# Kernel tuning notes

Measured on AMD Instinct MI355X. Metric: run time of the kernel, lower is better.

The kernel has to match this reference:

```python
import jax, jax.numpy as jnp
from jax import lax
import numpy as np

_LEVELS = [6 * 2 ** i for i in range(1, 8)]  # Dense size per block: 12..768
_LOG_2PI = float(np.log(2.0 * np.pi))


def _expm(A):
    # Differentiable matrix exponential: scaling-and-squaring + Taylor.
    K = 6
    A = A / (2.0 ** K)
    n = A.shape[-1]
    out = jnp.eye(n, dtype=A.dtype)
    term = out
    for j in range(1, 14):
        term = (term @ A) / j
        out = out + term
    for _ in range(K):
        out = out @ out
    return out


def _s2d(x):
    # tf.nn.space_to_depth, block_size=2, NHWC layout (channel order i*2*C+j*C+c)
    B, H, W, C = x.shape
    x = x.reshape(B, H // 2, 2, W // 2, 2, C).transpose(0, 1, 3, 2, 4, 5)
    return x.reshape(B, H // 2, W // 2, 4 * C)


def _block_inverse(y, M, eb, cw, cb, dw, db):
    # inverse of Block = Chain([Dense(s), RealNVP(s//2, shift-only)])
    # Dense inverse: expm(-M) @ (y - bias)
    x = jnp.einsum('ij,bhwj->bhwi', _expm(-M), y - eb)
    d = M.shape[0] // 2
    x0, x1 = x[..., :d], x[..., d:]
    # shift_and_log_scale: Dense(zeros-init) o relu(Conv2D(256,3,same)); scale=None
    h = jax.nn.relu(lax.conv_general_dilated(
        x0, cw, (1, 1), 'SAME', dimension_numbers=('NHWC', 'HWIO', 'NHWC')) + cb)
    shift = jnp.einsum('bhwk,kd->bhwd', h, dw) + db
    return jnp.concatenate([x0, x1 - shift], axis=-1)


def _log_prob(sample, params):
    x = sample
    ildj = jnp.zeros((), sample.dtype)
    for i, p in enumerate(params):  # levels i=1..7, applied in inverse order
        x = _s2d(x)                 # [B, 256/2^i, 256/2^i, 3*4^i]
        s = _LEVELS[i]
        blk = _block_inverse(x[..., :s], *p)
        x = blk if x.shape[-1] == s else jnp.concatenate([blk, x[..., s:]], axis=-1)
        H = x.shape[1]
        # Faithful to source: the Inline bijector's inverse_log_det_jacobian fn
        # literally returns exp(trace(M)) (a constant-Jacobian scalar), which TFP
        # reduces over the excess spatial event dims => multiply by H*W.
        ildj = ildj + jnp.exp(jnp.trace(p[0])) * (H * H)
    z = x.reshape(x.shape[0], -1)   # Reshape bijector inverse: flatten event
    N = z.shape[-1]
    base = -0.5 * jnp.sum(z * z, axis=-1) - 0.5 * N * _LOG_2PI
    return base + ildj


def setup_inputs() -> dict:
    key = jax.random.key(0)
    inp = {'sample': jax.random.normal(jax.random.fold_in(key, 0), (8, 256, 256, 3), jnp.float32)}
    for i in range(1, 8):
        s = 6 * 2 ** i
        d = s // 2
        ks = jax.random.split(jax.random.fold_in(key, i), 3)
        inp[f'M{i}'] = 0.05 * jax.random.normal(ks[0], (s, s), jnp.float32)
        inp[f'eb{i}'] = jnp.zeros((s,), jnp.float32)
        inp[f'cw{i}'] = jax.random.normal(ks[1], (3, 3, d, 256), jnp.float32) / np.sqrt(9.0 * d)
        inp[f'cb{i}'] = jnp.zeros((256,), jnp.float32)
        inp[f'dw{i}'] = 0.01 * jax.random.normal(ks[2], (256, d), jnp.float32)
        inp[f'db{i}'] = jnp.zeros((d,), jnp.float32)
    return inp


def reference(sample, M1, eb1, cw1, cb1, dw1, db1, M2, eb2, cw2, cb2, dw2, db2,
              M3, eb3, cw3, cb3, dw3, db3, M4, eb4, cw4, cb4, dw4, db4,
              M5, eb5, cw5, cb5, dw5, db5, M6, eb6, cw6, cb6, dw6, db6,
              M7, eb7, cw7, cb7, dw7, db7):
    params = [
        (M1, eb1, cw1, cb1, dw1, db1), (M2, eb2, cw2, cb2, dw2, db2),
        (M3, eb3, cw3, cb3, dw3, db3), (M4, eb4, cw4, cb4, dw4, db4),
        (M5, eb5, cw5, cb5, dw5, db5), (M6, eb6, cw6, cb6, dw6, db6),
        (M7, eb7, cw7, cb7, dw7, db7),
    ]
    return _log_prob(sample, params)
```

## Files before the change

### kernel.cpp

```cpp
#include <hip/hip_runtime.h>
#include <hip/hip_bf16.h>
#include <math.h>


#define NXEL 1572864

typedef __attribute__((ext_vector_type(8))) short bf16x8;
typedef __attribute__((ext_vector_type(4))) float f32x4;

__device__ inline unsigned pkbf(float a, float b) {
  union { __hip_bfloat16 h; unsigned short u; } ca, cb2;
  ca.h = __float2bfloat16(a);
  cb2.h = __float2bfloat16(b);
  return (unsigned)ca.u | ((unsigned)cb2.u << 16);
}

__global__ __launch_bounds__(256) void prep_all_kernel(
    const float* __restrict__ M1, const float* __restrict__ M2,
    const float* __restrict__ M3, const float* __restrict__ M4,
    const float* __restrict__ M5, const float* __restrict__ M6,
    const float* __restrict__ M7, const float* __restrict__ cw1,
    const float* __restrict__ cw2, const float* __restrict__ dw1,
    const float* __restrict__ dw2, float* __restrict__ MT,
    __hip_bfloat16* __restrict__ MTB, float* __restrict__ TR,
    __hip_bfloat16* __restrict__ CWT1, __hip_bfloat16* __restrict__ CWT2,
    __hip_bfloat16* __restrict__ DWT1, __hip_bfloat16* __restrict__ DWT2) {
  int bid = blockIdx.x, tid = threadIdx.x;
  if (bid < 48) {
    int idx = bid * 256 + tid;
    if (idx < 12240) {
      const int cum[5] = {0, 144, 720, 3024, 12240};
      int l = 0;
      while (idx >= cum[l + 1]) l++;
      int local = idx - cum[l];
      int s = 12 << l;
      int k = local / s, c = local - k * s;
      const float* Mp = l == 0 ? M1 : l == 1 ? M2 : l == 2 ? M3 : M4;
      MT[idx] = -Mp[c * s + k];
    }
  } else if (bid < 3072) {
    int idx = (bid - 48) * 256 + tid;
    if (idx < 774144) {
      const int cum[4] = {0, 36864, 184320, 774144};
      int l = 0;
      while (idx >= cum[l + 1]) l++;
      const float* Mp = l == 0 ? M5 : l == 1 ? M6 : M7;
      MTB[idx] = __float2bfloat16(-Mp[idx - cum[l]]);
    }
  } else if (bid < 3079) {
    __shared__ float red[256];
    int l = bid - 3072;
    const float* Mp = l == 0 ? M1 : l == 1 ? M2 : l == 2 ? M3 : l == 3 ? M4
                    : l == 4 ? M5 : l == 5 ? M6 : M7;
    int s = 12 << l;
    float su = 0.f;
    for (int i = tid; i < s; i += 256) su += Mp[(long)i * s + i];
    red[tid] = su;
    __syncthreads();
    for (int st = 128; st > 0; st >>= 1) {
      if (tid < st) red[tid] += red[tid + st];
      __syncthreads();
    }
    if (tid == 0) TR[l] = red[0];
  } else if (bid < 3143) {
    int idx = (bid - 3079) * 256 + tid;
    int n = idx >> 6, k = idx & 63;
    CWT1[idx] = __float2bfloat16(k < 54 ? cw1[k * 256 + n] : 0.f);
  } else if (bid < 3271) {
    int idx = (bid - 3143) * 256 + tid;
    int n = idx >> 7, k = idx & 127;
    CWT2[idx] = __float2bfloat16(k < 108 ? cw2[k * 256 + n] : 0.f);
  } else if (bid < 3287) {
    int idx = (bid - 3271) * 256 + tid;
    int c = idx >> 8, k = idx & 255;
    DWT1[idx] = __float2bfloat16(c < 6 ? dw1[k * 6 + c] : 0.f);
  } else {
    int idx = (bid - 3287) * 256 + tid;
    int c = idx >> 8, k = idx & 255;
    DWT2[idx] = __float2bfloat16(c < 12 ? dw2[k * 12 + c] : 0.f);
  }
}

__global__ __launch_bounds__(256) void expm_apply_kernel(
    const float* __restrict__ prev, const float* __restrict__ Mt,
    const float* __restrict__ eb, float* __restrict__ xblk,
    int s, int Cp, int h, int J, int tvs) {
  extern __shared__ float lds[];
  float* MtS = lds;
  float* Tb = lds + s * s;
  for (int i = threadIdx.x; i < s * s; i += 256) MtS[i] = Mt[i];

  int TV = 1 << tvs;
  int v = threadIdx.x >> tvs;
  int p = threadIdx.x & (TV - 1);
  int c0 = p * 6;
  int NV = 256 >> tvs;
  int sp = s + 1;
  int vec = blockIdx.x * NV + v;
  int hw = h * h;
  int b = vec / hw, rem = vec - b * hw;
  int y = rem / h, x = rem - (rem / h) * h;
  int W2 = 2 * h;
  long rowbase = ((long)(b * W2 + 2 * y) * W2 + 2 * x) * Cp;

  float acc[6];
#pragma unroll
  for (int m = 0; m < 6; m++) {
    int c = c0 + m;
    int q = c / Cp, cp = c - q * Cp;
    float xv = prev[rowbase + (long)((q >> 1) * W2 + (q & 1)) * Cp + cp] - eb[c];
    acc[m] = xv;
    Tb[v * sp + c0 + m] = xv;
  }
  __syncthreads();

  for (int j = 1; j <= J; j++) {
    float inv = 1.0f / (float)j;
    float tn[6] = {0.f, 0.f, 0.f, 0.f, 0.f, 0.f};
    const float* Trow = Tb + v * sp;
    for (int k = 0; k < s; k++) {
      float tv = Trow[k];
      const float* mrow = MtS + k * s + c0;
#pragma unroll
      for (int m = 0; m < 6; m++) tn[m] = fmaf(mrow[m], tv, tn[m]);
    }
    __syncthreads();
#pragma unroll
    for (int m = 0; m < 6; m++) {
      float t2 = tn[m] * inv;
      acc[m] += t2;
      Tb[v * sp + c0 + m] = t2;
    }
    __syncthreads();
  }

  float* xo = xblk + (long)vec * s;
#pragma unroll
  for (int m = 0; m < 6; m++) xo[c0 + m] = acc[m];
}

template <int S>
__global__ __launch_bounds__(S, 2) void expm_chain_kernel(
    const float* __restrict__ prev, const __hip_bfloat16* __restrict__ Mrow,
    const float* __restrict__ eb, float* __restrict__ xblk,
    int Cp, int h, int J) {
  constexpr int NU4 = S / 8;
  __shared__ float tbuf[2][S];
  int c = threadIdx.x;
  int vec = blockIdx.x;
  int hw = h * h, W2 = 2 * h;
  int b = vec / hw, rem = vec - b * hw;
  int y = rem / h, x = rem - (rem / h) * h;
  int q = c / Cp, cp = c - q * Cp;
  long a = ((long)(b * W2 + 2 * y + (q >> 1)) * W2 + 2 * x + (q & 1)) * Cp + cp;

  uint4 mreg[NU4];
  const uint4* rp = (const uint4*)(Mrow + (long)c * S);
#pragma unroll
  for (int k8 = 0; k8 < NU4; k8++) mreg[k8] = rp[k8];

  float v = prev[a] - eb[c];
  float acc = v;
  tbuf[0][c] = v;
  __syncthreads();

  int cur = 0;
  for (int j = 1; j <= J; j++) {
    float inv = 1.0f / (float)j;
    float sacc[4] = {0.f, 0.f, 0.f, 0.f};
    const float* t = tbuf[cur];
#pragma unroll
    for (int k8 = 0; k8 < NU4; k8++) {
      uint4 u = mreg[k8];
      const float* tt = t + (k8 << 3);
      float ss = sacc[k8 & 3];
      ss = fmaf(__uint_as_float(u.x << 16), tt[0], ss);
      ss = fmaf(__uint_as_float(u.x & 0xffff0000u), tt[1], ss);
      ss = fmaf(__uint_as_float(u.y << 16), tt[2], ss);
      ss = fmaf(__uint_as_float(u.y & 0xffff0000u), tt[3], ss);
      ss = fmaf(__uint_as_float(u.z << 16), tt[4], ss);
      ss = fmaf(__uint_as_float(u.z & 0xffff0000u), tt[5], ss);
      ss = fmaf(__uint_as_float(u.w << 16), tt[6], ss);
      ss = fmaf(__uint_as_float(u.w & 0xffff0000u), tt[7], ss);
      sacc[k8 & 3] = ss;
    }
    float tn = ((sacc[0] + sacc[1]) + (sacc[2] + sacc[3])) * inv;
    acc += tn;
    cur ^= 1;
    tbuf[cur][c] = tn;
    __syncthreads();
  }
  xblk[(long)vec * S + c] = acc;
}

__global__ __launch_bounds__(64) void expm_init_kernel(
    const float* __restrict__ prev, const float* __restrict__ eb,
    float* __restrict__ tcur, float* __restrict__ acc, int s, int Cp, int h,
    int nvec) {
  int total = nvec * s;
  int hw = h * h, W2 = 2 * h;
  for (int idx = blockIdx.x * 64 + threadIdx.x; idx < total;
       idx += gridDim.x * 64) {
    int v = idx / s, c = idx - (idx / s) * s;
    int b = v / hw, rem = v - b * hw;
    int y = rem / h, x = rem - (rem / h) * h;
    int q = c / Cp, cp = c - q * Cp;
    long a = ((long)(b * W2 + 2 * y + (q >> 1)) * W2 + 2 * x + (q & 1)) * Cp + cp;
    float xv = prev[a] - eb[c];
    tcur[idx] = xv;
    acc[idx] = xv;
  }
}

template <int S>
__global__ __launch_bounds__(64) void taylor_term_kernel(
    const __hip_bfloat16* __restrict__ Mrow, const float* __restrict__ t_old,
    float* __restrict__ t_new, float* __restrict__ acc, float inv_j) {
  __shared__ float tv[S];
  int tid = threadIdx.x;
  int v = blockIdx.y;
  int c = blockIdx.x * 64 + tid;
  const float4* t4 = (const float4*)(t_old + (long)v * S);
  float4* l4 = (float4*)tv;
  for (int i = tid; i < S / 4; i += 64) l4[i] = t4[i];
  __syncthreads();

  const uint4* rp = (const uint4*)(Mrow + (long)c * S);
  float sacc[4] = {0.f, 0.f, 0.f, 0.f};
#pragma unroll
  for (int k8 = 0; k8 < S / 8; k8++) {
    uint4 u = rp[k8];
    const float* tt = tv + (k8 << 3);
    float ss = sacc[k8 & 3];
    ss = fmaf(__uint_as_float(u.x << 16), tt[0], ss);
    ss = fmaf(__uint_as_float(u.x & 0xffff0000u), tt[1], ss);
    ss = fmaf(__uint_as_float(u.y << 16), tt[2], ss);
    ss = fmaf(__uint_as_float(u.y & 0xffff0000u), tt[3], ss);
    ss = fmaf(__uint_as_float(u.z << 16), tt[4], ss);
    ss = fmaf(__uint_as_float(u.z & 0xffff0000u), tt[5], ss);
    ss = fmaf(__uint_as_float(u.w << 16), tt[6], ss);
    ss = fmaf(__uint_as_float(u.w & 0xffff0000u), tt[7], ss);
    sacc[k8 & 3] = ss;
  }
  float tn = ((sacc[0] + sacc[1]) + (sacc[2] + sacc[3])) * inv_j;
  long o = (long)v * S + c;
  t_new[o] = tn;
  acc[o] += tn;
}

template <int D, int KSTEPS>
__global__ __launch_bounds__(256, 3) void conv_dense_mfma(
    const float* __restrict__ xblk, float* __restrict__ xout,
    const __hip_bfloat16* __restrict__ cwT, const float* __restrict__ cb,
    const __hip_bfloat16* __restrict__ dwT, const float* __restrict__ db,
    const float* __restrict__ prev, int h, int s, int Cfull, int Cp, int pass) {
  constexpr int K9 = 9 * D;
  constexpr int KP = KSTEPS * 32;
  constexpr int KS = KP + 8;
  constexpr int HS = 264;
  extern __shared__ __hip_bfloat16 uls[];
  __hip_bfloat16* A = uls;
  __hip_bfloat16* H = uls + 64 * KS;
  float* cbS = (float*)(uls + 64 * KS + 64 * HS);

  int w = h;
  int tilesX = w >> 3;
  int bt = blockIdx.x;
  int tx = bt % tilesX; int t1 = bt / tilesX;
  int ty = t1 % tilesX; int b = t1 / tilesX;
  int y0 = ty * 8, x0 = tx * 8;
  int tid = threadIdx.x;

  cbS[tid] = cb[tid];

#pragma unroll
  for (int it = 0; it < 3; ++it) {
    int idx = it * 256 + tid;
    if (idx < 576) {
      int m = idx / 9, t = idx - m * 9;
      int ky = t / 3, kx = t - ky * 3;
      int pr = m >> 3, pc = m & 7;
      int iy = y0 + pr + ky - 1, ix = x0 + pc + kx - 1;
      unsigned* dst = (unsigned*)&A[m * KS + t * D];
      if (iy >= 0 && iy < h && ix >= 0 && ix < w) {
        const float* src = &xblk[((long)((b * h + iy) * w + ix)) * s];
        if constexpr (D == 6) {
          float4 p0 = *(const float4*)src;
          float2 p1 = *(const float2*)(src + 4);
          dst[0] = pkbf(p0.x, p0.y);
          dst[1] = pkbf(p0.z, p0.w);
          dst[2] = pkbf(p1.x, p1.y);
        } else {
          float4 p0 = ((const float4*)src)[0];
          float4 p1 = ((const float4*)src)[1];
          float4 p2 = ((const float4*)src)[2];
          dst[0] = pkbf(p0.x, p0.y);
          dst[1] = pkbf(p0.z, p0.w);
          dst[2] = pkbf(p1.x, p1.y);
          dst[3] = pkbf(p1.z, p1.w);
          dst[4] = pkbf(p2.x, p2.y);
          dst[5] = pkbf(p2.z, p2.w);
        }
      } else {
#pragma unroll
        for (int j = 0; j < D / 2; j++) dst[j] = 0u;
      }
    }
  }
  constexpr int PADU = (KP - K9) / 2;
  for (int idx = tid; idx < 64 * PADU; idx += 256) {
    int m = idx / PADU, j = idx - m * PADU;
    ((unsigned*)&A[m * KS + K9])[j] = 0u;
  }
  __syncthreads();

  int wid = tid >> 6, lane = tid & 63;
  int ln = lane & 15, hi = lane >> 4;

  bf16x8 af[KSTEPS];
#pragma unroll
  for (int ks = 0; ks < KSTEPS; ks++)
    af[ks] = *(const bf16x8*)&A[(wid * 16 + ln) * KS + ks * 32 + hi * 8];

  const __hip_bfloat16* cwrow = cwT + ln * KP + hi * 8;
  bf16x8 bq[KSTEPS], bn[KSTEPS];
#pragma unroll
  for (int ks = 0; ks < KSTEPS; ks++)
    bq[ks] = *(const bf16x8*)&cwrow[ks * 32];
#pragma unroll 1
  for (int nt = 0; nt < 16; nt++) {
    if (nt < 15) {
#pragma unroll
      for (int ks = 0; ks < KSTEPS; ks++)
        bn[ks] = *(const bf16x8*)&cwrow[(nt + 1) * 16 * KP + ks * 32];
    }
    f32x4 acc = {0.f, 0.f, 0.f, 0.f};
#pragma unroll
    for (int ks = 0; ks < KSTEPS; ks++)
      acc = __builtin_amdgcn_mfma_f32_16x16x32_bf16(af[ks], bq[ks], acc, 0, 0, 0);
    float cbv = cbS[nt * 16 + ln];
#pragma unroll
    for (int r = 0; r < 4; r++) {
      float hv = fmaxf(acc[r] + cbv, 0.f);
      H[(wid * 16 + hi * 4 + r) * HS + nt * 16 + ln] = __float2bfloat16(hv);
    }
#pragma unroll
    for (int ks = 0; ks < KSTEPS; ks++) bq[ks] = bn[ks];
  }
  __syncthreads();

  f32x4 acc2 = {0.f, 0.f, 0.f, 0.f};
  const __hip_bfloat16* dwrow = dwT + ln * 256 + hi * 8;
#pragma unroll
  for (int ks = 0; ks < 8; ks++) {
    bf16x8 a2 = *(const bf16x8*)&H[(wid * 16 + ln) * HS + ks * 32 + hi * 8];
    bf16x8 b2 = *(const bf16x8*)&dwrow[ks * 32];
    acc2 = __builtin_amdgcn_mfma_f32_16x16x32_bf16(a2, b2, acc2, 0, 0, 0);
  }

  if (ln < D) {
    float dbv = db[ln];
#pragma unroll
    for (int r = 0; r < 4; r++) {
      int m = wid * 16 + hi * 4 + r;
      int pr = m >> 3, pc = m & 7;
      long pix = (long)((b * h + y0 + pr) * w + (x0 + pc));
      float sh = acc2[r] + dbv;
      float x0v = xblk[pix * s + ln];
      float x1v = xblk[pix * s + D + ln];
      xout[pix * Cfull + ln] = x0v;
      xout[pix * Cfull + D + ln] = x1v - sh;
    }
  }

  if (pass > 0) {
    int W2 = 2 * h;
    int nq = pass / Cp;
    int q0 = s / Cp;
    int tasks = 64 * nq;
    for (int idx = tid; idx < tasks; idx += 256) {
      int m = idx / nq, qi = idx - (idx / nq) * nq;
      int q = q0 + qi;
      int pr = m >> 3, pc = m & 7;
      int yy = y0 + pr, xx = x0 + pc;
      const float4* src = (const float4*)
          &prev[((long)(b * W2 + 2 * yy + (q >> 1)) * W2 + 2 * xx + (q & 1)) * Cp];
      float4* dst = (float4*)&xout[((long)((b * h + yy) * w + xx)) * Cfull + q * Cp];
      for (int j = 0; j < Cp / 4; j++) dst[j] = src[j];
    }
  }
}

template <int TH, int TW, int D>
__global__ __launch_bounds__(256) void conv_dense_v3(
    const float* __restrict__ xblk, float* __restrict__ xout,
    const float* __restrict__ cw, const float* __restrict__ cb,
    const float* __restrict__ dw, const float* __restrict__ db,
    const float* __restrict__ prev, int h, int s, int Cfull, int Cp, int pass) {
  constexpr int P = TH * TW;
  constexpr int PW = 8;
  constexpr int DP = D + 1;
  extern __shared__ float lds[];
  float* dwS = lds;
  float* hbufS = dwS + 256 * DP;
  float* scratch = hbufS + P * 257;
  float* patchS = scratch;

  int w = h;
  int tilesX = w / TW, tilesY = h / TH;
  int bt = blockIdx.x;
  int tx = bt % tilesX; int t1 = bt / tilesX;
  int ty = t1 % tilesY; int b = t1 / tilesY;
  int y0 = ty * TH, x0 = tx * TW;
  int tid = threadIdx.x;

  for (int idx = tid; idx < 256 * D; idx += 256) {
    int k = idx / D, c = idx % D;
    dwS[k * DP + c] = dw[idx];
  }

  constexpr int PATCHN = D * (TH + 2) * (TW + 2);
  for (int idx = tid; idx < PATCHN; idx += 256) {
    int ci = idx % D; int rest = idx / D;
    int px = rest % (TW + 2); int py = rest / (TW + 2);
    int iy = y0 + py - 1, ix = x0 + px - 1;
    float v = 0.f;
    if (iy >= 0 && iy < h && ix >= 0 && ix < w)
      v = xblk[((long)((b * h + iy) * w + ix)) * s + ci];
    patchS[(ci * (TH + 2) + py) * PW + px] = v;
  }
  __syncthreads();

  float acc[P];
  float cbk = cb[tid];
#pragma unroll
  for (int p = 0; p < P; p++) acc[p] = cbk;

  float wv[9];
#pragma unroll
  for (int t = 0; t < 9; t++) wv[t] = cw[(long)(t * D) * 256 + tid];

#pragma unroll 1
  for (int ci = 0; ci < D; ci++) {
    float wvn[9];
    if (ci + 1 < D) {
#pragma unroll
      for (int t = 0; t < 9; t++) wvn[t] = cw[(long)(t * D + ci + 1) * 256 + tid];
    }
    float r[TH + 2][6];
#pragma unroll
    for (int py = 0; py < TH + 2; py++) {
      const float* rp = &patchS[(ci * (TH + 2) + py) * PW];
#pragma unroll
      for (int u = 0; u < 6; u++) r[py][u] = rp[u];
    }
#pragma unroll
    for (int ky = 0; ky < 3; ky++)
#pragma unroll
      for (int kx = 0; kx < 3; kx++)
#pragma unroll
        for (int pr = 0; pr < TH; pr++)
#pragma unroll
          for (int pc = 0; pc < TW; pc++)
            acc[pr * TW + pc] =
                fmaf(r[pr + ky][pc + kx], wv[ky * 3 + kx], acc[pr * TW + pc]);
#pragma unroll
    for (int t = 0; t < 9; t++) wv[t] = wvn[t];
  }
#pragma unroll
  for (int p = 0; p < P; p++) hbufS[p * 257 + tid] = fmaxf(acc[p], 0.f);
  __syncthreads();

  {
    int p = tid & 15, kc = tid >> 4;
    float part[D];
#pragma unroll
    for (int c = 0; c < D; c++) part[c] = 0.f;
    const float* hrow = hbufS + p * 257 + kc * 16;
#pragma unroll
    for (int k = 0; k < 16; k++) {
      float hv = hrow[k];
      const float* dr = dwS + (kc * 16 + k) * DP;
#pragma unroll
      for (int c = 0; c < D; c++) part[c] = fmaf(hv, dr[c], part[c]);
    }
    __syncthreads();
    float* partial = scratch;
#pragma unroll
    for (int c = 0; c < D; c++) partial[(kc * 16 + p) * DP + c] = part[c];
  }
  __syncthreads();

  for (int idx = tid; idx < P * D; idx += 256) {
    int p = idx / D, c = idx % D;
    float sh = db[c];
    const float* pp = scratch + p * DP + c;
#pragma unroll
    for (int kc = 0; kc < 16; kc++) sh += pp[kc * 16 * DP];
    int pr = p / TW, pc = p % TW;
    long pix = (long)((b * h + y0 + pr) * w + (x0 + pc));
    float x0v = xblk[pix * s + c];
    float x1v = xblk[pix * s + D + c];
    xout[pix * Cfull + c] = x0v;
    xout[pix * Cfull + D + c] = x1v - sh;
  }

  if (pass > 0) {
    int W2 = 2 * h;
    for (int idx = tid; idx < P * pass; idx += 256) {
      int pp = idx / pass, c = 2 * D + idx - (idx / pass) * pass;
      int pr = pp / TW, pc = pp - (pp / TW) * TW;
      int yy = y0 + pr, xx = x0 + pc;
      int q = c / Cp, cp = c - q * Cp;
      long a = ((long)(b * W2 + 2 * yy + (q >> 1)) * W2 + 2 * xx + (q & 1)) * Cp + cp;
      xout[((long)((b * h + yy) * w + xx)) * Cfull + c] = prev[a];
    }
  }
}

template <int PIX>
__global__ __launch_bounds__(256) void conv_part_kernel(
    const float* __restrict__ xblk, const float* __restrict__ cw,
    float* __restrict__ hbuf, int h, int d, int s, int chunk) {
  extern __shared__ float pt[];
  int w = h;
  int nine_d = 9 * d;
  int j0 = blockIdx.y * chunk;
  int j1 = min(j0 + chunk, nine_d);
  int clen = j1 - j0;
  int pg = blockIdx.x;
  int tid = threadIdx.x;

  for (int idx = tid; idx < PIX * clen; idx += 256) {
    int q = idx / clen, jj = idx % clen;
    int j = j0 + jj;
    int t = j / d, ci = j - t * d;
    int ky = t / 3, kx = t % 3;
    int p = pg * PIX + q;
    int b = p / (h * w); int rem = p - b * h * w;
    int y = rem / w, x = rem - y * w;
    int iy = y + ky - 1, ix = x + kx - 1;
    float v = 0.f;
    if (iy >= 0 && iy < h && ix >= 0 && ix < w)
      v = xblk[((long)((b * h + iy) * w + ix)) * s + ci];
    pt[idx] = v;
  }
  __syncthreads();

  float acc[PIX];
#pragma unroll
  for (int q = 0; q < PIX; q++) acc[q] = 0.f;
  const float* cwp = cw + (long)j0 * 256 + tid;
#pragma unroll 4
  for (int jj = 0; jj < clen; jj++) {
    float cwv = cwp[(long)jj * 256];
#pragma unroll
    for (int q = 0; q < PIX; q++) acc[q] = fmaf(pt[q * clen + jj], cwv, acc[q]);
  }
#pragma unroll
  for (int q = 0; q < PIX; q++)
    atomicAdd(&hbuf[((long)(pg * PIX + q)) * 256 + tid], acc[q]);
}

__global__ __launch_bounds__(256) void dense_shift_kernel(
    const float* __restrict__ xblk, const float* __restrict__ hbuf,
    float* __restrict__ xout, const float* __restrict__ dw,
    const float* __restrict__ db, const float* __restrict__ cb,
    const float* __restrict__ prev, int d, int s, int Cfull, int Cp, int pass,
    int h, int nvec) {
  __shared__ float cbS[256];
  cbS[threadIdx.x] = cb[threadIdx.x];
  __syncthreads();
  int shiftN = nvec * d;
  for (int gid = blockIdx.x * 256 + threadIdx.x; gid < shiftN;
       gid += gridDim.x * 256) {
    int p = gid / d, c = gid - (gid / d) * d;
    float sum = db[c];
    const float* hrow = hbuf + (long)p * 256;
#pragma unroll 4
    for (int k = 0; k < 256; k++)
      sum = fmaf(fmaxf(hrow[k] + cbS[k], 0.f), dw[(long)k * d + c], sum);
    long pix = p;
    float x0v = xblk[pix * s + c];
    float x1v = xblk[pix * s + d + c];
    xout[pix * Cfull + c] = x0v;
    xout[pix * Cfull + d + c] = x1v - sum;
  }
  int hw = h * h, W2 = 2 * h;
  long passT = (long)nvec * pass;
  for (long e = blockIdx.x * 256 + threadIdx.x; e < passT;
       e += (long)gridDim.x * 256) {
    int p = (int)(e / pass);
    int c = s + (int)(e - (long)p * pass);
    int b = p / hw, rem = p - b * hw;
    int y = rem / h, x = rem - (rem / h) * h;
    int q = c / Cp, cp = c - q * Cp;
    long a = ((long)(b * W2 + 2 * y + (q >> 1)) * W2 + 2 * x + (q & 1)) * Cp + cp;
    xout[(long)p * Cfull + c] = prev[a];
  }
}

__global__ __launch_bounds__(256) void sumsq_kernel(const float* __restrict__ x,
                                                    float* __restrict__ part) {
  __shared__ float red[256];
  int b = blockIdx.x >> 6, ch = blockIdx.x & 63;
  const float* p = x + (long)b * 196608 + ch * 3072;
  float su = 0.f;
  for (int i = threadIdx.x; i < 3072; i += 256) {
    float v = p[i];
    su = fmaf(v, v, su);
  }
  red[threadIdx.x] = su;
  __syncthreads();
  for (int st = 128; st > 0; st >>= 1) {
    if (threadIdx.x < st) red[threadIdx.x] += red[threadIdx.x + st];
    __syncthreads();
  }
  if (threadIdx.x == 0) part[blockIdx.x] = red[0];
}

__global__ __launch_bounds__(256) void finalize_kernel(
    const float* __restrict__ part, const float* __restrict__ TR,
    float* __restrict__ out) {
  int tid = threadIdx.x;
  if (tid < 8) {
    float su = 0.f;
    for (int c = 0; c < 64; c++) su += part[tid * 64 + c];
    float ildj = 0.f;
    const float Hsq[7] = {16384.f, 4096.f, 1024.f, 256.f, 64.f, 16.f, 4.f};
#pragma unroll
    for (int i = 0; i < 7; i++) ildj += expf(TR[i]) * Hsq[i];
    out[tid] = -0.5f * su - 0.5f * 196608.0f * 1.8378770664093453f + ildj;
  }
}

extern "C" void kernel_launch(void* const* d_in, const int* in_sizes, int n_in,
                              void* d_out, int out_size, void* d_ws, size_t ws_size,
                              hipStream_t stream) {
  (void)in_sizes; (void)n_in; (void)out_size;
  const size_t need =
      ((size_t)3 * NXEL + 2 * 98304 + 387072 + 8 + 512) * sizeof(float);
  if (ws_size < need) return;

  const float* sample = (const float*)d_in[0];
  float* ws = (float*)d_ws;
  float* Xa = ws;
  float* Xb = Xa + NXEL;
  float* XBLK = Xb + NXEL;
  float* HBUF = XBLK + 262144;
  float* TCUR = XBLK + NXEL;
  float* MT = TCUR;
  __hip_bfloat16* CWT1 = (__hip_bfloat16*)(TCUR + 12240);
  __hip_bfloat16* CWT2 = (__hip_bfloat16*)(TCUR + 20432);
  __hip_bfloat16* DWT1 = (__hip_bfloat16*)(TCUR + 36816);
  __hip_bfloat16* DWT2 = (__hip_bfloat16*)(TCUR + 38864);
  float* TNXT = TCUR + 98304;
  __hip_bfloat16* MTB = (__hip_bfloat16*)(TNXT + 98304);
  float* TR = (float*)(MTB + 774144);
  float* PART = TR + 8;
  float* out = (float*)d_out;

  const float* Mp[7];
  const float *ebp[7], *cwp[7], *cbp[7], *dwp[7], *dbp[7];
  for (int i = 0; i < 7; i++) {
    Mp[i] = (const float*)d_in[1 + 6 * i + 0];
    ebp[i] = (const float*)d_in[1 + 6 * i + 1];
    cwp[i] = (const float*)d_in[1 + 6 * i + 2];
    cbp[i] = (const float*)d_in[1 + 6 * i + 3];
    dwp[i] = (const float*)d_in[1 + 6 * i + 4];
    dbp[i] = (const float*)d_in[1 + 6 * i + 5];
  }

  prep_all_kernel<<<3303, 256, 0, stream>>>(
      Mp[0], Mp[1], Mp[2], Mp[3], Mp[4], Mp[5], Mp[6], cwp[0], cwp[1], dwp[0],
      dwp[1], MT, MTB, TR, CWT1, CWT2, DWT1, DWT2);

  const int Jarr[7] = {5, 5, 6, 7, 7, 8, 10};
  const int MTOFF[4] = {0, 144, 720, 3024};
  const int MTBOFF[3] = {0, 36864, 184320};
  const int PIXa[7] = {0, 0, 0, 8, 8, 4, 2};
  const int KCa[7] = {0, 0, 0, 4, 16, 32, 64};

  int C = 3;
  for (int i = 0; i < 7; i++) {
    int s = 12 << i, d = s >> 1, h = 128 >> i;
    int Cp = C;
    int Cfull = 4 * C;
    int pass = Cfull - s;
    int nvec = 8 * h * h;
    float* xs2d = (i & 1) ? Xb : Xa;
    const float* prev = (i == 0) ? sample : ((i & 1) ? Xa : Xb);

    if (s <= 96) {
      int tvs = i + 1;
      int NV = 256 >> tvs;
      int ldsB = (s * s + NV * (s + 1)) * 4;
      expm_apply_kernel<<<nvec / NV, 256, ldsB, stream>>>(
          prev, MT + MTOFF[i], ebp[i], XBLK, s, Cp, h, Jarr[i], tvs);
    } else if (i == 4) {
      expm_chain_kernel<192><<<nvec, 192, 0, stream>>>(
          prev, MTB + MTBOFF[0], ebp[i], XBLK, Cp, h, Jarr[i]);
    } else {
      expm_init_kernel<<<384, 64, 0, stream>>>(prev, ebp[i], TCUR, XBLK, s, Cp,
                                               h, nvec);
      float* ta = TCUR;
      float* tb = TNXT;
      dim3 g(s / 64, nvec);
      for (int j = 1; j <= Jarr[i]; j++) {
        if (i == 5)
          taylor_term_kernel<384><<<g, 64, 0, stream>>>(
              MTB + MTBOFF[1], ta, tb, XBLK, 1.0f / (float)j);
        else
          taylor_term_kernel<768><<<g, 64, 0, stream>>>(
              MTB + MTBOFF[2], ta, tb, XBLK, 1.0f / (float)j);
        float* tmp = ta; ta = tb; tb = tmp;
      }
    }

    if (i == 0) {
      int blocks = 8 * (h / 8) * (h / 8);
      int ldsB = (64 * (64 + 8) + 64 * 264) * 2 + 1024;
      conv_dense_mfma<6, 2><<<blocks, 256, ldsB, stream>>>(
          XBLK, xs2d, CWT1, cbp[0], DWT1, dbp[0], prev, h, s, Cfull, Cp, pass);
    } else if (i == 1) {
      int blocks = 8 * (h / 8) * (h / 8);
      int ldsB = (64 * (128 + 8) + 64 * 264) * 2 + 1024;
      conv_dense_mfma<12, 4><<<blocks, 256, ldsB, stream>>>(
          XBLK, xs2d, CWT2, cbp[1], DWT2, dbp[1], prev, h, s, Cfull, Cp, pass);
    } else if (i == 2) {
      int blocks = 8 * (h / 4) * (h / 4);
      int ldsB = (2 * 256 * (d + 1) + 16 * 257) * 4;
      conv_dense_v3<4, 4, 24><<<blocks, 256, ldsB, stream>>>(
          XBLK, xs2d, cwp[i], cbp[i], dwp[i], dbp[i], prev, h, s, Cfull, Cp, pass);
    } else {
      hipMemsetAsync(HBUF, 0, (size_t)nvec * 256 * 4, stream);
      int PIX = PIXa[i], KC = KCa[i];
      int nine_d = 9 * d;
      int chunk = (nine_d + KC - 1) / KC;
      dim3 ga(nvec / PIX, KC);
      int alds = PIX * chunk * 4;
      if (PIX == 8)
        conv_part_kernel<8><<<ga, 256, alds, stream>>>(XBLK, cwp[i], HBUF, h, d, s, chunk);
      else if (PIX == 4)
        conv_part_kernel<4><<<ga, 256, alds, stream>>>(XBLK, cwp[i], HBUF, h, d, s, chunk);
      else
        conv_part_kernel<2><<<ga, 256, alds, stream>>>(XBLK, cwp[i], HBUF, h, d, s, chunk);
      long shiftN = (long)nvec * d, passT = (long)nvec * pass;
      int dsb = (int)((shiftN + 255) / 256 + (passT + 255) / 256);
      if (dsb > 4096) dsb = 4096;
      dense_shift_kernel<<<dsb, 256, 0, stream>>>(
          XBLK, HBUF, xs2d, dwp[i], dbp[i], cbp[i], prev, d, s, Cfull, Cp, pass,
          h, nvec);
    }
    C = Cfull;
  }

  sumsq_kernel<<<512, 256, 0, stream>>>(Xa, PART);
  finalize_kernel<<<1, 256, 0, stream>>>(PART, TR, out);
}
```

Before: 488.5 us.

## Fuse 1x1 dense into conv epilogue with FP32 register accumulation and shuffles

```diff
diff --git a/kernel.cpp b/kernel.cpp
--- a/kernel.cpp
+++ b/kernel.cpp
@@ -20,11 +20,9 @@
     const float* __restrict__ M3, const float* __restrict__ M4,
     const float* __restrict__ M5, const float* __restrict__ M6,
     const float* __restrict__ M7, const float* __restrict__ cw1,
-    const float* __restrict__ cw2, const float* __restrict__ dw1,
-    const float* __restrict__ dw2, float* __restrict__ MT,
+    const float* __restrict__ cw2, float* __restrict__ MT,
     __hip_bfloat16* __restrict__ MTB, float* __restrict__ TR,
-    __hip_bfloat16* __restrict__ CWT1, __hip_bfloat16* __restrict__ CWT2,
-    __hip_bfloat16* __restrict__ DWT1, __hip_bfloat16* __restrict__ DWT2) {
+    __hip_bfloat16* __restrict__ CWT1, __hip_bfloat16* __restrict__ CWT2) {
   int bid = blockIdx.x, tid = threadIdx.x;
   if (bid < 48) {
     int idx = bid * 256 + tid;
@@ -66,18 +64,10 @@
     int idx = (bid - 3079) * 256 + tid;
     int n = idx >> 6, k = idx & 63;
     CWT1[idx] = __float2bfloat16(k < 54 ? cw1[k * 256 + n] : 0.f);
-  } else if (bid < 3271) {
+  } else {
     int idx = (bid - 3143) * 256 + tid;
     int n = idx >> 7, k = idx & 127;
     CWT2[idx] = __float2bfloat16(k < 108 ? cw2[k * 256 + n] : 0.f);
-  } else if (bid < 3287) {
-    int idx = (bid - 3271) * 256 + tid;
-    int c = idx >> 8, k = idx & 255;
-    DWT1[idx] = __float2bfloat16(c < 6 ? dw1[k * 6 + c] : 0.f);
-  } else {
-    int idx = (bid - 3287) * 256 + tid;
-    int c = idx >> 8, k = idx & 255;
-    DWT2[idx] = __float2bfloat16(c < 12 ? dw2[k * 12 + c] : 0.f);
   }
 }
 
@@ -249,19 +239,18 @@
 }
 
 template <int D, int KSTEPS>
-__global__ __launch_bounds__(256, 3) void conv_dense_mfma(
+__global__ __launch_bounds__(256) void conv_dense_mfma(
     const float* __restrict__ xblk, float* __restrict__ xout,
     const __hip_bfloat16* __restrict__ cwT, const float* __restrict__ cb,
-    const __hip_bfloat16* __restrict__ dwT, const float* __restrict__ db,
+    const float* __restrict__ dw, const float* __restrict__ db,
     const float* __restrict__ prev, int h, int s, int Cfull, int Cp, int pass) {
   constexpr int K9 = 9 * D;
   constexpr int KP = KSTEPS * 32;
   constexpr int KS = KP + 8;
-  constexpr int HS = 264;
   extern __shared__ __hip_bfloat16 uls[];
   __hip_bfloat16* A = uls;
-  __hip_bfloat16* H = uls + 64 * KS;
-  float* cbS = (float*)(uls + 64 * KS + 64 * HS);
+  float* dwS = (float*)(uls + 64 * KS);
+  float* cbS = dwS + 256 * D;
 
   int w = h;
   int tilesX = w >> 3;
@@ -271,6 +260,7 @@
   int y0 = ty * 8, x0 = tx * 8;
   int tid = threadIdx.x;
 
+  for (int idx = tid; idx < 256 * D; idx += 256) dwS[idx] = dw[idx];
   cbS[tid] = cb[tid];
 
 #pragma unroll
@@ -327,6 +317,13 @@
 #pragma unroll
   for (int ks = 0; ks < KSTEPS; ks++)
     bq[ks] = *(const bf16x8*)&cwrow[ks * 32];
+
+  float part[4][D];
+#pragma unroll
+  for (int r = 0; r < 4; r++)
+#pragma unroll
+    for (int c = 0; c < D; c++) part[r][c] = 0.f;
+
 #pragma unroll 1
   for (int nt = 0; nt < 16; nt++) {
     if (nt < 15) {
@@ -338,39 +335,44 @@
 #pragma unroll
     for (int ks = 0; ks < KSTEPS; ks++)
       acc = __builtin_amdgcn_mfma_f32_16x16x32_bf16(af[ks], bq[ks], acc, 0, 0, 0);
-    float cbv = cbS[nt * 16 + ln];
+    int k = nt * 16 + ln;
+    float cbv = cbS[k];
+    const float* dr = dwS + k * D;
 #pragma unroll
     for (int r = 0; r < 4; r++) {
       float hv = fmaxf(acc[r] + cbv, 0.f);
-      H[(wid * 16 + hi * 4 + r) * HS + nt * 16 + ln] = __float2bfloat16(hv);
+#pragma unroll
+      for (int c = 0; c < D; c++) part[r][c] = fmaf(hv, dr[c], part[r][c]);
     }
 #pragma unroll
     for (int ks = 0; ks < KSTEPS; ks++) bq[ks] = bn[ks];
   }
-  __syncthreads();
-
-  f32x4 acc2 = {0.f, 0.f, 0.f, 0.f};
-  const __hip_bfloat16* dwrow = dwT + ln * 256 + hi * 8;
-#pragma unroll
-  for (int ks = 0; ks < 8; ks++) {
-    bf16x8 a2 = *(const bf16x8*)&H[(wid * 16 + ln) * HS + ks * 32 + hi * 8];
-    bf16x8 b2 = *(const bf16x8*)&dwrow[ks * 32];
-    acc2 = __builtin_amdgcn_mfma_f32_16x16x32_bf16(a2, b2, acc2, 0, 0, 0);
-  }
-
-  if (ln < D) {
-    float dbv = db[ln];
+
+#pragma unroll
+  for (int msk = 1; msk <= 8; msk <<= 1)
+#pragma unroll
+    for (int r = 0; r < 4; r++)
+#pragma unroll
+      for (int c = 0; c < D; c++)
+        part[r][c] += __shfl_xor(part[r][c], msk, 64);
+
+  if (ln == 0) {
 #pragma unroll
     for (int r = 0; r < 4; r++) {
       int m = wid * 16 + hi * 4 + r;
       int pr = m >> 3, pc = m & 7;
       long pix = (long)((b * h + y0 + pr) * w + (x0 + pc));
-      float sh = acc2[r] + dbv;
-      float x0v = xblk[pix * s + ln];
-      float x1v = xblk[pix * s + D + ln];
-      xout[pix * Cfull + ln] = x0v;
-      xout[pix * Cfull + D + ln] = x1v - sh;
-    }
+#pragma unroll
+      for (int c = 0; c < D; c++)
+        xout[pix * Cfull + D + c] = xblk[pix * s + D + c] - (part[r][c] + db[c]);
+    }
+  }
+
+  for (int idx = tid; idx < 64 * D; idx += 256) {
+    int m = idx / D, c = idx - (idx / D) * D;
+    int pr = m >> 3, pc = m & 7;
+    long pix = (long)((b * h + y0 + pr) * w + (x0 + pc));
+    xout[pix * Cfull + c] = xblk[pix * s + c];
   }
 
   if (pass > 0) {
@@ -652,8 +654,6 @@
   float* MT = TCUR;
   __hip_bfloat16* CWT1 = (__hip_bfloat16*)(TCUR + 12240);
   __hip_bfloat16* CWT2 = (__hip_bfloat16*)(TCUR + 20432);
-  __hip_bfloat16* DWT1 = (__hip_bfloat16*)(TCUR + 36816);
-  __hip_bfloat16* DWT2 = (__hip_bfloat16*)(TCUR + 38864);
   float* TNXT = TCUR + 98304;
   __hip_bfloat16* MTB = (__hip_bfloat16*)(TNXT + 98304);
   float* TR = (float*)(MTB + 774144);
@@ -671,9 +671,9 @@
     dbp[i] = (const float*)d_in[1 + 6 * i + 5];
   }
 
-  prep_all_kernel<<<3303, 256, 0, stream>>>(
-      Mp[0], Mp[1], Mp[2], Mp[3], Mp[4], Mp[5], Mp[6], cwp[0], cwp[1], dwp[0],
-      dwp[1], MT, MTB, TR, CWT1, CWT2, DWT1, DWT2);
+  prep_all_kernel<<<3271, 256, 0, stream>>>(
+      Mp[0], Mp[1], Mp[2], Mp[3], Mp[4], Mp[5], Mp[6], cwp[0], cwp[1], MT, MTB,
+      TR, CWT1, CWT2);
 
   const int Jarr[7] = {5, 5, 6, 7, 7, 8, 10};
   const int MTOFF[4] = {0, 144, 720, 3024};
@@ -719,14 +719,14 @@
 
     if (i == 0) {
       int blocks = 8 * (h / 8) * (h / 8);
-      int ldsB = (64 * (64 + 8) + 64 * 264) * 2 + 1024;
+      int ldsB = 64 * (64 + 8) * 2 + (256 * 6 + 256) * 4;
       conv_dense_mfma<6, 2><<<blocks, 256, ldsB, stream>>>(
-          XBLK, xs2d, CWT1, cbp[0], DWT1, dbp[0], prev, h, s, Cfull, Cp, pass);
+          XBLK, xs2d, CWT1, cbp[0], dwp[0], dbp[0], prev, h, s, Cfull, Cp, pass);
     } else if (i == 1) {
       int blocks = 8 * (h / 8) * (h / 8);
-      int ldsB = (64 * (128 + 8) + 64 * 264) * 2 + 1024;
+      int ldsB = 64 * (128 + 8) * 2 + (256 * 12 + 256) * 4;
       conv_dense_mfma<12, 4><<<blocks, 256, ldsB, stream>>>(
-          XBLK, xs2d, CWT2, cbp[1], DWT2, dbp[1], prev, h, s, Cfull, Cp, pass);
+          XBLK, xs2d, CWT2, cbp[1], dwp[1], dbp[1], prev, h, s, Cfull, Cp, pass);
     } else if (i == 2) {
       int blocks = 8 * (h / 4) * (h / 4);
       int ldsB = (2 * 256 * (d + 1) + 16 * 257) * 4;
```

After: 487.7 us. About the same (-0.2%).
